# Optimization experiments

Hardware: AMD Instinct MI355X
Metric: run time of the kernel (lower is better)

## Reference

```python
import jax, jax.numpy as jnp
import numpy as np

B, LL, LP, D, H, TOPK = 4, 256, 256, 256, 128, 100


def setup_inputs() -> dict:
    key = jax.random.key(0)
    ks = jax.random.split(key, 16)
    s = 0.02
    return {
        "l_tok": jax.random.normal(ks[0], (B, LL, D), jnp.float32),
        "p_tok": jax.random.normal(ks[1], (B, LP, D), jnp.float32),
        "l_pad": jax.random.bernoulli(ks[2], 0.1, (B, LL)),
        "p_pad": jax.random.bernoulli(ks[3], 0.1, (B, LP)),
        "Wl": jax.random.normal(ks[4], (D, D), jnp.float32) * s,
        "bl": jnp.zeros((D,), jnp.float32),
        "Wp": jax.random.normal(ks[5], (D, D), jnp.float32) * s,
        "bp": jnp.zeros((D,), jnp.float32),
        "W1": jax.random.normal(ks[6], (H, 4 * D), jnp.float32) * s,
        "b1": jnp.zeros((H,), jnp.float32),
        "W2": jax.random.normal(ks[7], (H, H), jnp.float32) * s,
        "b2": jnp.zeros((H,), jnp.float32),
        "W3": jax.random.normal(ks[8], (1, H), jnp.float32) * s,
        "b3": jnp.zeros((1,), jnp.float32),
    }


def reference(l_tok, p_tok, l_pad, p_pad, Wl, bl, Wp, bp, W1, b1, W2, b2, W3, b3):
    # Linear projections (torch Linear: x @ W.T + b)
    l = jnp.einsum("bld,ed->ble", l_tok, Wl) + bl  # [B,Ll,D]
    p = jnp.einsum("bpd,ed->bpe", p_tok, Wp) + bp  # [B,Lp,D]

    le = jnp.broadcast_to(l[:, :, None, :], (B, LL, LP, D))
    pe = jnp.broadcast_to(p[:, None, :, :], (B, LL, LP, D))
    pair_feat = jnp.concatenate([le, pe, le * pe, jnp.abs(le - pe)], axis=-1)  # [B,Ll,Lp,4D]

    gelu = lambda x: jax.nn.gelu(x, approximate=False)  # torch nn.GELU default (erf)
    h = gelu(jnp.einsum("blpf,hf->blph", pair_feat, W1) + b1)
    h = gelu(jnp.einsum("blph,gh->blpg", h, W2) + b2)
    pair_logit = (jnp.einsum("blph,oh->blpo", h, W3) + b3)[..., 0]  # [B,Ll,Lp]

    pair_logit = jnp.nan_to_num(pair_logit, nan=0.0, posinf=20.0, neginf=-20.0)

    valid = (~l_pad)[:, :, None] & (~p_pad)[:, None, :]  # [B,Ll,Lp]
    pair_logit = jnp.where(valid, pair_logit, -20.0)
    pair_prob = jax.nn.sigmoid(pair_logit)

    flat = pair_logit.reshape(B, -1)
    k_top = min(TOPK, LL * LP)
    topv, _ = jax.lax.top_k(flat, k_top)  # [B,k]
    w = jax.nn.softmax(topv, axis=-1)
    logit = jnp.sum(w * topv, axis=-1)  # [B]
    return logit, pair_logit, pair_prob
```

## Files before the change

### kernel.cpp

```cpp
#include <hip/hip_runtime.h>

#define BB 4
#define LLL 256
#define LPP 256
#define DDIM 256
#define HH 128

typedef _Float16 f16;
typedef f16 f16x8 __attribute__((ext_vector_type(8)));
typedef f16 f16x4 __attribute__((ext_vector_type(4)));
typedef float floatx4 __attribute__((ext_vector_type(4)));

__device__ __forceinline__ float gelu_f(float x) {
    return x * __builtin_amdgcn_rcpf(1.f + __expf(-1.702f * x));
}
__device__ __forceinline__ float sigmoid_f(float x) {
    return __builtin_amdgcn_rcpf(1.f + __expf(-x));
}
__device__ __forceinline__ f16x8 habs8(f16x8 v) {
    uint4 u = __builtin_bit_cast(uint4, v);
    u.x &= 0x7fff7fffu; u.y &= 0x7fff7fffu; u.z &= 0x7fff7fffu; u.w &= 0x7fff7fffu;
    return __builtin_bit_cast(f16x8, u);
}
__device__ __forceinline__ unsigned okey(float f) {
    unsigned u = __float_as_uint(f);
    return (u & 0x80000000u) ? ~u : (u | 0x80000000u);
}

#define TK_H0(b) (tk + (b) * 256)
#define TK_H1(b) (tk + 1024 + (b) * 256)
#define TK_S1(b) ((float*)(tk + 2048) + (b))
#define TK_S2(b) ((float*)(tk + 2052) + (b))
#define TK_CNT(b) (tk + 2056 + (b))
#define TK_INTS 2060

__global__ __launch_bounds__(256) void prep_proj(
    const float* __restrict__ l_tok, const float* __restrict__ p_tok,
    const float* __restrict__ Wl, const float* __restrict__ Wp,
    const float* __restrict__ bl, const float* __restrict__ bp,
    f16* __restrict__ proj) {
    __shared__ __align__(16) char sm[2 * 64 * 80];
    f16* As = (f16*)sm;
    f16* Bs = (f16*)(sm + 64 * 80);
    int tid = threadIdx.x;
    int m0 = blockIdx.x * 64, n0 = blockIdx.y * 64;
    bool isP = (m0 >= 1024);
    const float* Asrc = isP ? (p_tok + (size_t)(m0 - 1024) * DDIM) : (l_tok + (size_t)m0 * DDIM);
    const float* Wsrc = isP ? Wp : Wl;
    const float* bias = isP ? bp : bl;
    int row = tid >> 2, seg = tid & 3;
    int w = tid >> 6, lane = tid & 63;
    int m16 = lane & 15, quad = lane >> 4;
    int wm = w & 1, wn = w >> 1;
    floatx4 acc[2][2];
#pragma unroll
    for (int a = 0; a < 2; ++a)
#pragma unroll
        for (int c = 0; c < 2; ++c) acc[a][c] = (floatx4)0.f;
    for (int k0 = 0; k0 < DDIM; k0 += 32) {
        float4 f0 = *(const float4*)(Asrc + row * DDIM + k0 + seg * 8);
        float4 f1 = *(const float4*)(Asrc + row * DDIM + k0 + seg * 8 + 4);
        f16x8 av;
        av[0] = (f16)f0.x; av[1] = (f16)f0.y; av[2] = (f16)f0.z; av[3] = (f16)f0.w;
        av[4] = (f16)f1.x; av[5] = (f16)f1.y; av[6] = (f16)f1.z; av[7] = (f16)f1.w;
        *(f16x8*)(As + row * 40 + seg * 8) = av;
        float4 g0 = *(const float4*)(Wsrc + (n0 + row) * DDIM + k0 + seg * 8);
        float4 g1 = *(const float4*)(Wsrc + (n0 + row) * DDIM + k0 + seg * 8 + 4);
        f16x8 bv;
        bv[0] = (f16)g0.x; bv[1] = (f16)g0.y; bv[2] = (f16)g0.z; bv[3] = (f16)g0.w;
        bv[4] = (f16)g1.x; bv[5] = (f16)g1.y; bv[6] = (f16)g1.z; bv[7] = (f16)g1.w;
        *(f16x8*)(Bs + row * 40 + seg * 8) = bv;
        __syncthreads();
        f16x8 afr[2], bfr[2];
#pragma unroll
        for (int t = 0; t < 2; ++t)
            afr[t] = *(const f16x8*)(As + (wm * 32 + t * 16 + m16) * 40 + quad * 8);
#pragma unroll
        for (int t = 0; t < 2; ++t)
            bfr[t] = *(const f16x8*)(Bs + (wn * 32 + t * 16 + m16) * 40 + quad * 8);
#pragma unroll
        for (int a = 0; a < 2; ++a)
#pragma unroll
            for (int c = 0; c < 2; ++c)
                acc[a][c] = __builtin_amdgcn_mfma_f32_16x16x32_f16(afr[a], bfr[c], acc[a][c], 0, 0, 0);
        __syncthreads();
    }
#pragma unroll
    for (int c = 0; c < 2; ++c) {
        int col = n0 + wn * 32 + c * 16 + m16;
        float bv = bias[col];
#pragma unroll
        for (int a = 0; a < 2; ++a) {
            int rbase = m0 + wm * 32 + a * 16 + quad * 4;
#pragma unroll
            for (int i = 0; i < 4; ++i)
                proj[(size_t)(rbase + i) * DDIM + col] = (f16)(acc[a][c][i] + bv);
        }
    }
}

__global__ __launch_bounds__(256) void prep_ab(
    const f16* __restrict__ proj, const float* __restrict__ W1,
    const float* __restrict__ W2, float* __restrict__ ABt,
    f16* __restrict__ w1g, f16* __restrict__ w2g, int* __restrict__ tk) {
    int tid = threadIdx.x;
    if (blockIdx.x >= 32) {
        int idx = ((blockIdx.x - 32) * 2 + blockIdx.y) * 256 + tid;
        if (idx < 8192) {
            int m16 = idx & 15, quad = (idx >> 4) & 3, th = (idx >> 6) & 7;
            int cd = (idx >> 9) & 1, ds = idx >> 10;
            int h = th * 16 + m16;
            const float* src = W1 + (size_t)h * 1024 + 512 + cd * 256 + ds * 32 + quad * 8;
            f16x8 v;
#pragma unroll
            for (int j = 0; j < 8; ++j) v[j] = (f16)src[j];
            *(f16x8*)(w1g + (size_t)idx * 8) = v;
        } else if (idx < 8192 + 2048) {
            int c = idx - 8192;
            int m16 = c & 15, quad = (c >> 4) & 3, tg = (c >> 6) & 7, ks = c >> 9;
            int g = tg * 16 + m16;
            f16x8 v;
#pragma unroll
            for (int j = 0; j < 8; ++j) v[j] = (f16)W2[g * HH + j * 16 + ks * 4 + quad];
            *(f16x8*)(w2g + (size_t)c * 8) = v;
        } else {
            int zid = idx - 10240;
            if (zid >= 0 && zid < TK_INTS) tk[zid] = 0;
        }
        return;
    }
    __shared__ __align__(16) char sm[2 * 64 * 80];
    f16* As = (f16*)sm;
    f16* Bs = (f16*)(sm + 64 * 80);
    int m0 = blockIdx.x * 64, n0 = blockIdx.y * 64;
    bool isP = (m0 >= 1024);
    int koff = isP ? 256 : 0;
    int row = tid >> 2, seg = tid & 3;
    int w = tid >> 6, lane = tid & 63;
    int m16 = lane & 15, quad = lane >> 4;
    int wm = w & 1, wn = w >> 1;
    floatx4 acc[2][2];
#pragma unroll
    for (int a = 0; a < 2; ++a)
#pragma unroll
        for (int c = 0; c < 2; ++c) acc[a][c] = (floatx4)0.f;
    for (int k0 = 0; k0 < DDIM; k0 += 32) {
        f16x8 av = *(const f16x8*)(proj + (size_t)(m0 + row) * DDIM + k0 + seg * 8);
        *(f16x8*)(As + row * 40 + seg * 8) = av;
        float4 g0 = *(const float4*)(W1 + (size_t)(n0 + row) * 1024 + koff + k0 + seg * 8);
        float4 g1 = *(const float4*)(W1 + (size_t)(n0 + row) * 1024 + koff + k0 + seg * 8 + 4);
        f16x8 bv;
        bv[0] = (f16)g0.x; bv[1] = (f16)g0.y; bv[2] = (f16)g0.z; bv[3] = (f16)g0.w;
        bv[4] = (f16)g1.x; bv[5] = (f16)g1.y; bv[6] = (f16)g1.z; bv[7] = (f16)g1.w;
        *(f16x8*)(Bs + row * 40 + seg * 8) = bv;
        __syncthreads();
        f16x8 afr[2], bfr[2];
#pragma unroll
        for (int t = 0; t < 2; ++t)
            afr[t] = *(const f16x8*)(As + (wm * 32 + t * 16 + m16) * 40 + quad * 8);
#pragma unroll
        for (int t = 0; t < 2; ++t)
            bfr[t] = *(const f16x8*)(Bs + (wn * 32 + t * 16 + m16) * 40 + quad * 8);
#pragma unroll
        for (int a = 0; a < 2; ++a)
#pragma unroll
            for (int c = 0; c < 2; ++c)
                acc[a][c] = __builtin_amdgcn_mfma_f32_16x16x32_f16(afr[a], bfr[c], acc[a][c], 0, 0, 0);
        __syncthreads();
    }
#pragma unroll
    for (int c = 0; c < 2; ++c) {
        int col = n0 + wn * 32 + c * 16 + m16;
#pragma unroll
        for (int a = 0; a < 2; ++a) {
            int rbase = m0 + wm * 32 + a * 16 + quad * 4;
#pragma unroll
            for (int i = 0; i < 4; ++i)
                ABt[(size_t)col * 2048 + rbase + i] = acc[a][c][i];
        }
    }
}

#define H1_STRIDE 272
#define SM_PLOG 139264
#define SM_HIST 141312
#define SM_TOTAL 142336

__global__ __launch_bounds__(512, 2) void pair_main(
    const f16* __restrict__ proj, const float* __restrict__ ABt,
    const f16* __restrict__ w1g, const f16* __restrict__ w2g,
    const float* __restrict__ b1, const float* __restrict__ b2,
    const float* __restrict__ W3, const float* __restrict__ b3,
    const int* __restrict__ l_pad, const int* __restrict__ p_pad,
    float* __restrict__ out, int* __restrict__ tk) {
    __shared__ __align__(16) char sm[SM_TOTAL];
    int tid = threadIdx.x;
    int lane = tid & 63, w = tid >> 6;
    int m16 = lane & 15, quad = lane >> 4;
    int wp = w & 3, wh = w >> 2;
    int p0 = wp * 64, h0 = wh * 64;
    int b = blockIdx.y;
    int l0 = blockIdx.x * 2;
    int ml0 = b * LLL + l0;
    float* outPL = out + 4;
    float* outPR = out + 4 + BB * LLL * LPP;

    bool pad0 = (l_pad[ml0] != 0), pad1 = (l_pad[ml0 + 1] != 0);
    if (pad0 && pad1) {
        float pr = sigmoid_f(-20.f);
        if (tid < 512) {
            int j = tid >> 8, p = tid & 255;
            outPL[(size_t)(ml0 + j) * LPP + p] = -20.f;
            outPR[(size_t)(ml0 + j) * LPP + p] = pr;
        }
        if (tid == 0) atomicAdd(&TK_H0(b)[okey(-20.f) >> 24], 512);
        return;
    }

    float* plog = (float*)(sm + SM_PLOG);
    int* lhist = (int*)(sm + SM_HIST);

#pragma unroll
    for (int r = 0; r < 16; ++r) {
        int c = tid + r * 512;
        *(f16x8*)(sm + c * 16) = *(const f16x8*)(w1g + (size_t)c * 8);
    }
    if (tid < 512) plog[tid] = 0.f;
    if (tid < 256) lhist[tid] = 0;

    floatx4 acc[2][4][4];
    {
        float av[2][4];
#pragma unroll
        for (int th = 0; th < 4; ++th) {
            int hh = h0 + th * 16 + m16;
            float base = b1[hh];
            av[0][th] = ABt[(size_t)hh * 2048 + ml0] + base;
            av[1][th] = ABt[(size_t)hh * 2048 + ml0 + 1] + base;
        }
#pragma unroll
        for (int tp = 0; tp < 4; ++tp) {
            int rp = p0 + tp * 16 + quad * 4;
#pragma unroll
            for (int th = 0; th < 4; ++th) {
                int hh = h0 + th * 16 + m16;
                floatx4 bp4 = *(const floatx4*)(ABt + (size_t)hh * 2048 + 1024 + b * LPP + rp);
#pragma unroll
                for (int j = 0; j < 2; ++j) {
                    floatx4 a;
#pragma unroll
                    for (int i = 0; i < 4; ++i) a[i] = bp4[i] + av[j][th];
                    acc[j][tp][th] = a;
                }
            }
        }
    }
    __syncthreads();

    {
        const f16* Lr0 = proj + (size_t)ml0 * DDIM + quad * 8;
        const f16* Lr1 = Lr0 + DDIM;
        const f16* Prl[4];
#pragma unroll
        for (int tp = 0; tp < 4; ++tp)
            Prl[tp] = proj + (size_t)(1024 + b * LPP + p0 + tp * 16 + m16) * DDIM + quad * 8;

        f16x8 lv0 = *(const f16x8*)(Lr0);
        f16x8 lv1 = *(const f16x8*)(Lr1);
        f16x8 pv[4];
#pragma unroll
        for (int tp = 0; tp < 4; ++tp) pv[tp] = *(const f16x8*)(Prl[tp]);

        for (int ds = 0; ds < 8; ++ds) {
            f16x8 nlv0, nlv1, npv[4];
            if (ds < 7) {
                nlv0 = *(const f16x8*)(Lr0 + (ds + 1) * 32);
                nlv1 = *(const f16x8*)(Lr1 + (ds + 1) * 32);
#pragma unroll
                for (int tp = 0; tp < 4; ++tp)
                    npv[tp] = *(const f16x8*)(Prl[tp] + (ds + 1) * 32);
            }
            const char* wb = sm + (size_t)(ds * 2) * 8192 + (wh * 4) * 1024 + quad * 256 + m16 * 16;
            {
                f16x8 x[2][4];
#pragma unroll
                for (int tp = 0; tp < 4; ++tp) {
                    x[0][tp] = lv0 * pv[tp];
                    x[1][tp] = lv1 * pv[tp];
                }
#pragma unroll
                for (int th = 0; th < 4; ++th) {
                    f16x8 bf = *(const f16x8*)(wb + th * 1024);
#pragma unroll
                    for (int j = 0; j < 2; ++j)
#pragma unroll
                        for (int tp = 0; tp < 4; ++tp)
                            acc[j][tp][th] = __builtin_amdgcn_mfma_f32_16x16x32_f16(x[j][tp], bf, acc[j][tp][th], 0, 0, 0);
                }
            }
            {
                f16x8 x[2][4];
#pragma unroll
                for (int tp = 0; tp < 4; ++tp) {
                    x[0][tp] = habs8(lv0 - pv[tp]);
                    x[1][tp] = habs8(lv1 - pv[tp]);
                }
#pragma unroll
                for (int th = 0; th < 4; ++th) {
                    f16x8 bf = *(const f16x8*)(wb + 8192 + th * 1024);
#pragma unroll
                    for (int j = 0; j < 2; ++j)
#pragma unroll
                        for (int tp = 0; tp < 4; ++tp)
                            acc[j][tp][th] = __builtin_amdgcn_mfma_f32_16x16x32_f16(x[j][tp], bf, acc[j][tp][th], 0, 0, 0);
                }
            }
            lv0 = nlv0; lv1 = nlv1;
#pragma unroll
            for (int tp = 0; tp < 4; ++tp) pv[tp] = npv[tp];
        }
    }
    __syncthreads();

#pragma unroll
    for (int j = 0; j < 2; ++j) {
        char* h1s = sm + j * (256 * H1_STRIDE);
#pragma unroll
        for (int tp = 0; tp < 4; ++tp) {
#pragma unroll
            for (int i = 0; i < 4; ++i) {
                f16x4 hv;
#pragma unroll
                for (int th = 0; th < 4; ++th) hv[th] = (f16)gelu_f(acc[j][tp][th][i]);
                int p = p0 + tp * 16 + quad * 4 + i;
                *(f16x4*)(h1s + p * H1_STRIDE + m16 * 16 + wh * 8) = hv;
            }
        }
    }
    __syncthreads();

    float b2v[4], w3v[4];
#pragma unroll
    for (int th = 0; th < 4; ++th) {
        int g = h0 + th * 16 + m16;
        b2v[th] = b2[g];
        w3v[th] = W3[g];
    }
    floatx4 acc2[2][4][4];
#pragma unroll
    for (int j = 0; j < 2; ++j)
#pragma unroll
        for (int tp = 0; tp < 4; ++tp)
#pragma unroll
            for (int th = 0; th < 4; ++th) {
                floatx4 a;
                a[0] = a[1] = a[2] = a[3] = b2v[th];
                acc2[j][tp][th] = a;
            }
#pragma unroll
    for (int ks = 0; ks < 4; ++ks) {
        f16x8 af[2][4];
#pragma unroll
        for (int j = 0; j < 2; ++j)
#pragma unroll
            for (int tp = 0; tp < 4; ++tp)
                af[j][tp] = *(const f16x8*)(sm + j * (256 * H1_STRIDE) +
                                            (p0 + tp * 16 + m16) * H1_STRIDE + ks * 64 + quad * 16);
#pragma unroll
        for (int th = 0; th < 4; ++th) {
            f16x8 bf = *(const f16x8*)(w2g + (size_t)(((ks * 8 + wh * 4 + th) * 4 + quad) * 16 + m16) * 8);
#pragma unroll
            for (int j = 0; j < 2; ++j)
#pragma unroll
                for (int tp = 0; tp < 4; ++tp)
                    acc2[j][tp][th] = __builtin_amdgcn_mfma_f32_16x16x32_f16(af[j][tp], bf, acc2[j][tp][th], 0, 0, 0);
        }
    }

#pragma unroll
    for (int j = 0; j < 2; ++j) {
        float part[16];
#pragma unroll
        for (int q = 0; q < 16; ++q) part[q] = 0.f;
#pragma unroll
        for (int tp = 0; tp < 4; ++tp)
#pragma unroll
            for (int th = 0; th < 4; ++th)
#pragma unroll
                for (int i = 0; i < 4; ++i)
                    part[tp * 4 + i] += w3v[th] * gelu_f(acc2[j][tp][th][i]);
#pragma unroll
        for (int mask = 1; mask <= 8; mask <<= 1)
#pragma unroll
            for (int q = 0; q < 16; ++q) part[q] += __shfl_xor(part[q], mask, 64);
        if (m16 == 0) {
#pragma unroll
            for (int tp = 0; tp < 4; ++tp)
#pragma unroll
                for (int i = 0; i < 4; ++i)
                    atomicAdd(&plog[j * 256 + p0 + tp * 16 + quad * 4 + i], part[tp * 4 + i]);
        }
    }
    __syncthreads();

    if (tid < 512) {
        int j = tid >> 8, p = tid & 255;
        int ml = ml0 + j;
        float pl;
        if (l_pad[ml] != 0) {
            pl = -20.f;
        } else {
            pl = plog[tid] + b3[0];
            if (__builtin_isnan(pl)) pl = 0.f;
            else if (__builtin_isinf(pl)) pl = pl > 0.f ? 20.f : -20.f;
            if (p_pad[b * LPP + p] != 0) pl = -20.f;
        }
        outPL[(size_t)ml * LPP + p] = pl;
        outPR[(size_t)ml * LPP + p] = sigmoid_f(pl);
        atomicAdd(&lhist[okey(pl) >> 24], 1);
    }
    __syncthreads();
    if (tid < 256 && lhist[tid]) atomicAdd(&TK_H0(b)[tid], lhist[tid]);
}

__global__ __launch_bounds__(256) void tk_pass1(const float* __restrict__ pl,
                                                int* __restrict__ tk) {
    __shared__ int s[257];
    __shared__ int h[256];
    __shared__ float red[8];
    int tid = threadIdx.x, b = blockIdx.y;
    int lane = tid & 63, wv = tid >> 6;
    s[tid] = TK_H0(b)[tid];
    h[tid] = 0;
    __syncthreads();
    for (int off = 1; off < 256; off <<= 1) {
        int v = (tid + off < 256) ? s[tid + off] : 0;
        __syncthreads();
        s[tid] += v;
        __syncthreads();
    }
    int nxt = (tid < 255) ? s[tid + 1] : 0;
    if (s[tid] >= 100 && nxt < 100) s[256] = tid;
    __syncthreads();
    unsigned pref0 = (unsigned)s[256];

    float4 t = ((const float4*)(pl + (size_t)b * 65536 + blockIdx.x * 1024))[tid];
    float s1 = 0.f, s2 = 0.f;
#pragma unroll
    for (int c = 0; c < 4; ++c) {
        float v = (&t.x)[c];
        unsigned key = okey(v);
        unsigned hi = key >> 24;
        if (hi > pref0) {
            float e = __expf(v);
            s1 += e;
            s2 += e * v;
        } else if (hi == pref0) {
            atomicAdd(&h[(key >> 16) & 255], 1);
        }
    }
    __syncthreads();
    if (h[tid]) atomicAdd(&TK_H1(b)[tid], h[tid]);
    for (int off = 32; off > 0; off >>= 1) {
        s1 += __shfl_xor(s1, off, 64);
        s2 += __shfl_xor(s2, off, 64);
    }
    if (lane == 0) { red[wv] = s1; red[4 + wv] = s2; }
    __syncthreads();
    if (tid == 0) {
        float a = red[0] + red[1] + red[2] + red[3];
        float bsum = red[4] + red[5] + red[6] + red[7];
        if (a != 0.f) {
            atomicAdd(TK_S1(b), a);
            atomicAdd(TK_S2(b), bsum);
        }
    }
}

__global__ __launch_bounds__(256) void tk_pass2(const float* __restrict__ pl,
                                                int* __restrict__ tk,
                                                float* __restrict__ out) {
    __shared__ int s[258];
    __shared__ float red[8];
    int tid = threadIdx.x, b = blockIdx.y;
    int lane = tid & 63, wv = tid >> 6;
    s[tid] = TK_H0(b)[tid];
    __syncthreads();
    for (int off = 1; off < 256; off <<= 1) {
        int v = (tid + off < 256) ? s[tid + off] : 0;
        __syncthreads();
        s[tid] += v;
        __syncthreads();
    }
    {
        int nxt = (tid < 255) ? s[tid + 1] : 0;
        if (s[tid] >= 100 && nxt < 100) { s[256] = tid; s[257] = 100 - nxt; }
    }
    __syncthreads();
    unsigned pref0 = (unsigned)s[256];
    int rem0 = s[257];
    __syncthreads();
    s[tid] = TK_H1(b)[tid];
    __syncthreads();
    for (int off = 1; off < 256; off <<= 1) {
        int v = (tid + off < 256) ? s[tid + off] : 0;
        __syncthreads();
        s[tid] += v;
        __syncthreads();
    }
    {
        int nxt = (tid < 255) ? s[tid + 1] : 0;
        if (s[tid] >= rem0 && nxt < rem0) { s[256] = tid; s[257] = rem0 - nxt; }
    }
    __syncthreads();
    unsigned pref1 = (unsigned)s[256];
    int rem1 = s[257];

    float4 t = ((const float4*)(pl + (size_t)b * 65536 + blockIdx.x * 1024))[tid];
    float s1 = 0.f, s2 = 0.f;
#pragma unroll
    for (int c = 0; c < 4; ++c) {
        float v = (&t.x)[c];
        unsigned key = okey(v);
        if ((key >> 24) == pref0 && ((key >> 16) & 255) > pref1) {
            float e = __expf(v);
            s1 += e;
            s2 += e * v;
        }
    }
    for (int off = 32; off > 0; off >>= 1) {
        s1 += __shfl_xor(s1, off, 64);
        s2 += __shfl_xor(s2, off, 64);
    }
    if (lane == 0) { red[wv] = s1; red[4 + wv] = s2; }
    __syncthreads();
    if (tid == 0) {
        float a = red[0] + red[1] + red[2] + red[3];
        float bsum = red[4] + red[5] + red[6] + red[7];
        if (a != 0.f) {
            atomicAdd(TK_S1(b), a);
            atomicAdd(TK_S2(b), bsum);
        }
        __threadfence();
        int done = atomicAdd(TK_CNT(b), 1);
        if (done == gridDim.x - 1) {
            float S1 = atomicAdd(TK_S1(b), 0.f);
            float S2 = atomicAdd(TK_S2(b), 0.f);
            unsigned key = (pref0 << 24) | (pref1 << 16) | 0x8000u;
            unsigned bits = (key & 0x80000000u) ? (key & 0x7fffffffu) : ~key;
            float vT = __uint_as_float(bits);
            float e = __expf(vT);
            S1 += (float)rem1 * e;
            S2 += (float)rem1 * e * vT;
            out[b] = S2 * __builtin_amdgcn_rcpf(S1);
        }
    }
}

extern "C" void kernel_launch(void* const* d_in, const int* in_sizes, int n_in,
                              void* d_out, int out_size, void* d_ws, size_t ws_size,
                              hipStream_t stream) {
    const float* l_tok = (const float*)d_in[0];
    const float* p_tok = (const float*)d_in[1];
    const int* l_pad = (const int*)d_in[2];
    const int* p_pad = (const int*)d_in[3];
    const float* Wl = (const float*)d_in[4];
    const float* bl = (const float*)d_in[5];
    const float* Wp = (const float*)d_in[6];
    const float* bp = (const float*)d_in[7];
    const float* W1 = (const float*)d_in[8];
    const float* b1 = (const float*)d_in[9];
    const float* W2 = (const float*)d_in[10];
    const float* b2 = (const float*)d_in[11];
    const float* W3 = (const float*)d_in[12];
    const float* b3 = (const float*)d_in[13];
    float* out = (float*)d_out;

    char* ws = (char*)d_ws;
    f16* proj = (f16*)ws;
    float* ABt = (float*)(ws + (size_t)2048 * 256 * 2);
    f16* w1g = (f16*)(ws + (size_t)2048 * 256 * 2 + (size_t)128 * 2048 * 4);
    f16* w2g = (f16*)((char*)w1g + (size_t)8192 * 16);
    int* tk = (int*)((char*)w2g + (size_t)2048 * 16);

    prep_proj<<<dim3(32, 4), 256, 0, stream>>>(l_tok, p_tok, Wl, Wp, bl, bp, proj);
    prep_ab<<<dim3(57, 2), 256, 0, stream>>>(proj, W1, W2, ABt, w1g, w2g, tk);
    pair_main<<<dim3(LLL / 2, BB), 512, 0, stream>>>(proj, ABt, w1g, w2g, b1, b2, W3, b3,
                                                     l_pad, p_pad, out, tk);
    const float* pl = out + 4;
    tk_pass1<<<dim3(64, BB), 256, 0, stream>>>(pl, tk);
    tk_pass2<<<dim3(64, BB), 256, 0, stream>>>(pl, tk, out);
}
```

Baseline: 178.9 us.

## Merge top-k passes into one kernel with grid-wide spin barriers

```diff
diff --git a/kernel.cpp b/kernel.cpp
--- a/kernel.cpp
+++ b/kernel.cpp
@@ -31,8 +31,10 @@
 #define TK_H1(b) (tk + 1024 + (b) * 256)
 #define TK_S1(b) ((float*)(tk + 2048) + (b))
 #define TK_S2(b) ((float*)(tk + 2052) + (b))
-#define TK_CNT(b) (tk + 2056 + (b))
-#define TK_INTS 2060
+#define TK_CA(b) (tk + 2056 + (b))
+#define TK_CB(b) (tk + 2060 + (b))
+#define TK_CC(b) (tk + 2064 + (b))
+#define TK_INTS 2068
 
 __global__ __launch_bounds__(256) void prep_proj(
     const float* __restrict__ l_tok, const float* __restrict__ p_tok,
@@ -183,8 +185,7 @@
 
 #define H1_STRIDE 272
 #define SM_PLOG 139264
-#define SM_HIST 141312
-#define SM_TOTAL 142336
+#define SM_TOTAL 141312
 
 __global__ __launch_bounds__(512, 2) void pair_main(
     const f16* __restrict__ proj, const float* __restrict__ ABt,
@@ -192,7 +193,7 @@
     const float* __restrict__ b1, const float* __restrict__ b2,
     const float* __restrict__ W3, const float* __restrict__ b3,
     const int* __restrict__ l_pad, const int* __restrict__ p_pad,
-    float* __restrict__ out, int* __restrict__ tk) {
+    float* __restrict__ out) {
     __shared__ __align__(16) char sm[SM_TOTAL];
     int tid = threadIdx.x;
     int lane = tid & 63, w = tid >> 6;
@@ -213,12 +214,10 @@
             outPL[(size_t)(ml0 + j) * LPP + p] = -20.f;
             outPR[(size_t)(ml0 + j) * LPP + p] = pr;
         }
-        if (tid == 0) atomicAdd(&TK_H0(b)[okey(-20.f) >> 24], 512);
         return;
     }
 
     float* plog = (float*)(sm + SM_PLOG);
-    int* lhist = (int*)(sm + SM_HIST);
 
 #pragma unroll
     for (int r = 0; r < 16; ++r) {
@@ -226,7 +225,6 @@
         *(f16x8*)(sm + c * 16) = *(const f16x8*)(w1g + (size_t)c * 8);
     }
     if (tid < 512) plog[tid] = 0.f;
-    if (tid < 256) lhist[tid] = 0;
 
     floatx4 acc[2][4][4];
     {
@@ -417,20 +415,33 @@
         }
         outPL[(size_t)ml * LPP + p] = pl;
         outPR[(size_t)ml * LPP + p] = sigmoid_f(pl);
-        atomicAdd(&lhist[okey(pl) >> 24], 1);
-    }
-    __syncthreads();
-    if (tid < 256 && lhist[tid]) atomicAdd(&TK_H0(b)[tid], lhist[tid]);
-}
-
-__global__ __launch_bounds__(256) void tk_pass1(const float* __restrict__ pl,
-                                                int* __restrict__ tk) {
-    __shared__ int s[257];
+    }
+}
+
+__global__ __launch_bounds__(256) void tk_all(const float* __restrict__ pl,
+                                              int* __restrict__ tk,
+                                              float* __restrict__ out) {
+    __shared__ int s[258];
     __shared__ int h[256];
     __shared__ float red[8];
     int tid = threadIdx.x, b = blockIdx.y;
     int lane = tid & 63, wv = tid >> 6;
-    s[tid] = TK_H0(b)[tid];
+    float4 t = ((const float4*)(pl + (size_t)b * 65536 + blockIdx.x * 1024))[tid];
+
+    h[tid] = 0;
+    __syncthreads();
+#pragma unroll
+    for (int c = 0; c < 4; ++c) atomicAdd(&h[okey((&t.x)[c]) >> 24], 1);
+    __syncthreads();
+    if (h[tid]) atomicAdd(&TK_H0(b)[tid], h[tid]);
+    __threadfence();
+    if (tid == 0) {
+        atomicAdd(TK_CA(b), 1);
+        while (atomicAdd(TK_CA(b), 0) < (int)gridDim.x) __builtin_amdgcn_s_sleep(2);
+    }
+    __syncthreads();
+
+    s[tid] = atomicAdd(&TK_H0(b)[tid], 0);
     h[tid] = 0;
     __syncthreads();
     for (int off = 1; off < 256; off <<= 1) {
@@ -439,12 +450,13 @@
         s[tid] += v;
         __syncthreads();
     }
-    int nxt = (tid < 255) ? s[tid + 1] : 0;
-    if (s[tid] >= 100 && nxt < 100) s[256] = tid;
+    {
+        int nxt = (tid < 255) ? s[tid + 1] : 0;
+        if (s[tid] >= 100 && nxt < 100) { s[256] = tid; s[257] = 100 - nxt; }
+    }
     __syncthreads();
     unsigned pref0 = (unsigned)s[256];
-
-    float4 t = ((const float4*)(pl + (size_t)b * 65536 + blockIdx.x * 1024))[tid];
+    int rem0 = s[257];
     float s1 = 0.f, s2 = 0.f;
 #pragma unroll
     for (int c = 0; c < 4; ++c) {
@@ -469,38 +481,18 @@
     __syncthreads();
     if (tid == 0) {
         float a = red[0] + red[1] + red[2] + red[3];
-        float bsum = red[4] + red[5] + red[6] + red[7];
+        float bs = red[4] + red[5] + red[6] + red[7];
         if (a != 0.f) {
             atomicAdd(TK_S1(b), a);
-            atomicAdd(TK_S2(b), bsum);
-        }
-    }
-}
-
-__global__ __launch_bounds__(256) void tk_pass2(const float* __restrict__ pl,
-                                                int* __restrict__ tk,
-                                                float* __restrict__ out) {
-    __shared__ int s[258];
-    __shared__ float red[8];
-    int tid = threadIdx.x, b = blockIdx.y;
-    int lane = tid & 63, wv = tid >> 6;
-    s[tid] = TK_H0(b)[tid];
-    __syncthreads();
-    for (int off = 1; off < 256; off <<= 1) {
-        int v = (tid + off < 256) ? s[tid + off] : 0;
-        __syncthreads();
-        s[tid] += v;
-        __syncthreads();
-    }
-    {
-        int nxt = (tid < 255) ? s[tid + 1] : 0;
-        if (s[tid] >= 100 && nxt < 100) { s[256] = tid; s[257] = 100 - nxt; }
-    }
-    __syncthreads();
-    unsigned pref0 = (unsigned)s[256];
-    int rem0 = s[257];
-    __syncthreads();
-    s[tid] = TK_H1(b)[tid];
+            atomicAdd(TK_S2(b), bs);
+        }
+        __threadfence();
+        atomicAdd(TK_CB(b), 1);
+        while (atomicAdd(TK_CB(b), 0) < (int)gridDim.x) __builtin_amdgcn_s_sleep(2);
+    }
+    __syncthreads();
+
+    s[tid] = atomicAdd(&TK_H1(b)[tid], 0);
     __syncthreads();
     for (int off = 1; off < 256; off <<= 1) {
         int v = (tid + off < 256) ? s[tid + off] : 0;
@@ -515,9 +507,7 @@
     __syncthreads();
     unsigned pref1 = (unsigned)s[256];
     int rem1 = s[257];
-
-    float4 t = ((const float4*)(pl + (size_t)b * 65536 + blockIdx.x * 1024))[tid];
-    float s1 = 0.f, s2 = 0.f;
+    s1 = 0.f; s2 = 0.f;
 #pragma unroll
     for (int c = 0; c < 4; ++c) {
         float v = (&t.x)[c];
@@ -536,14 +526,14 @@
     __syncthreads();
     if (tid == 0) {
         float a = red[0] + red[1] + red[2] + red[3];
-        float bsum = red[4] + red[5] + red[6] + red[7];
+        float bs = red[4] + red[5] + red[6] + red[7];
         if (a != 0.f) {
             atomicAdd(TK_S1(b), a);
-            atomicAdd(TK_S2(b), bsum);
+            atomicAdd(TK_S2(b), bs);
         }
         __threadfence();
-        int done = atomicAdd(TK_CNT(b), 1);
-        if (done == gridDim.x - 1) {
+        int done = atomicAdd(TK_CC(b), 1);
+        if (done == (int)gridDim.x - 1) {
             float S1 = atomicAdd(TK_S1(b), 0.f);
             float S2 = atomicAdd(TK_S2(b), 0.f);
             unsigned key = (pref0 << 24) | (pref1 << 16) | 0x8000u;
@@ -586,8 +576,6 @@
     prep_proj<<<dim3(32, 4), 256, 0, stream>>>(l_tok, p_tok, Wl, Wp, bl, bp, proj);
     prep_ab<<<dim3(57, 2), 256, 0, stream>>>(proj, W1, W2, ABt, w1g, w2g, tk);
     pair_main<<<dim3(LLL / 2, BB), 512, 0, stream>>>(proj, ABt, w1g, w2g, b1, b2, W3, b3,
-                                                     l_pad, p_pad, out, tk);
-    const float* pl = out + 4;
-    tk_pass1<<<dim3(64, BB), 256, 0, stream>>>(pl, tk);
-    tk_pass2<<<dim3(64, BB), 256, 0, stream>>>(pl, tk, out);
-}
+                                                     l_pad, p_pad, out);
+    tk_all<<<dim3(64, BB), 256, 0, stream>>>(out + 4, tk, out);
+}
```

Measured after the change: 207.3 us. 1.16x slower.
